# Kernel optimization log

Hardware: AMD Instinct MI355X
Metric: run time of the kernel (lower is better)

## Reference

```python
import jax, jax.numpy as jnp
import numpy as np

N_NODES = 100000
N_EDGES = 1600000
F_IN = 256
F_OUT = 128


def setup_inputs() -> dict:
    key = jax.random.key(0)
    k1, k2, k3, k4, k5 = jax.random.split(key, 5)
    x = jax.random.normal(k1, (N_NODES, F_IN), dtype=jnp.float32)
    edge_src = jax.random.randint(k2, (N_EDGES,), 0, N_NODES, dtype=jnp.int64)
    edge_dst = jax.random.randint(k3, (N_EDGES,), 0, N_NODES, dtype=jnp.int64)
    edge_vals = jax.random.uniform(k4, (N_EDGES,), dtype=jnp.float32)
    kernel = jax.random.normal(k5, (F_IN, F_OUT), dtype=jnp.float32) * (1.0 / np.sqrt(F_IN))
    bias = jnp.zeros((F_OUT,), dtype=jnp.float32)
    return {"x": x, "edge_src": edge_src, "edge_dst": edge_dst,
            "edge_vals": edge_vals, "kernel": kernel, "bias": bias}


def reference(x, edge_src, edge_dst, edge_vals, kernel, bias):
    # h = x @ kernel  (dense feature transform), [N, F_OUT]
    h = x @ kernel
    # output = adj @ h  (sparse aggregation over COO edges)
    # message for edge e: adj[dst, src] * h[src]
    msg = h[edge_src] * edge_vals[:, None]          # [E, F_OUT]
    out = jax.ops.segment_sum(msg, edge_dst, num_segments=N_NODES)
    return out + bias
```

## Files before the change

### kernel.cpp

```cpp
#include <hip/hip_runtime.h>

constexpr int F_IN  = 256;
constexpr int F_OUT = 128;

constexpr int BSHIFT = 6;
constexpr int SUPSH  = 5;
constexpr int NPSH   = BSHIFT + SUPSH;
constexpr int NPS    = 1 << NPSH;
constexpr int EPT    = 16;
constexpr int BATCH  = 256 * EPT;

typedef __attribute__((ext_vector_type(8))) short short8;
typedef __attribute__((ext_vector_type(4))) float f32x4;

__device__ __forceinline__ unsigned short f2bf(float f) {
    unsigned u = __float_as_uint(f);
    u += 0x7fffu + ((u >> 16) & 1u);
    return (unsigned short)(u >> 16);
}

__global__ void prep_wt_kernel(const float* __restrict__ W,
                               unsigned short* __restrict__ Wt,
                               int* __restrict__ cnt)
{
    int n = blockIdx.x;
    int k = threadIdx.x;
    int ks = k >> 5, kk = k & 31;
    Wt[((ks * F_OUT) + n) * 32 + kk] = f2bf(W[k * F_OUT + n]);
    if (blockIdx.x == 0 && threadIdx.x < 64) cnt[threadIdx.x] = 0;
}

#define BS_LD 40

__global__ __launch_bounds__(256) void gemm_mfma_kernel(
    const float* __restrict__ x, const unsigned short* __restrict__ Wt,
    unsigned short* __restrict__ h, int n_nodes)
{
    __shared__ unsigned short Bs[2][F_OUT * BS_LD];

    const int tid  = threadIdx.x;
    const int wave = tid >> 6;
    const int lane = tid & 63;
    const int m16  = lane & 15;
    const int quad = lane >> 4;
    const int k0q  = quad * 8;
    const int arow = blockIdx.x * 64 + wave * 16 + m16;
    const bool inb = arow < n_nodes;

    f32x4 acc[8];
    #pragma unroll
    for (int t = 0; t < 8; ++t) acc[t] = (f32x4)(0.f);

    {
        const uint4* wsrc = (const uint4*)Wt;
        #pragma unroll
        for (int p = 0; p < 2; ++p) {
            int c = p * 256 + tid;
            *(uint4*)&Bs[0][(c >> 2) * BS_LD + (c & 3) * 8] = wsrc[c];
        }
    }

    float4 a0 = make_float4(0.f,0.f,0.f,0.f), a1 = a0;
    if (inb) {
        a0 = *(const float4*)&x[(long long)arow * F_IN + k0q];
        a1 = *(const float4*)&x[(long long)arow * F_IN + k0q + 4];
    }
    __syncthreads();

    #pragma unroll
    for (int ks = 0; ks < 8; ++ks) {
        uint4 s0, s1;
        if (ks < 7) {
            const uint4* wsrc = (const uint4*)(Wt + (size_t)(ks + 1) * F_OUT * 32);
            s0 = wsrc[tid];
            s1 = wsrc[256 + tid];
        }

        short8 af;
        af[0] = (short)f2bf(a0.x); af[1] = (short)f2bf(a0.y);
        af[2] = (short)f2bf(a0.z); af[3] = (short)f2bf(a0.w);
        af[4] = (short)f2bf(a1.x); af[5] = (short)f2bf(a1.y);
        af[6] = (short)f2bf(a1.z); af[7] = (short)f2bf(a1.w);
        if (!inb) af = (short8)0;

        if (ks < 7 && inb) {
            int kn = (ks + 1) * 32 + k0q;
            a0 = *(const float4*)&x[(long long)arow * F_IN + kn];
            a1 = *(const float4*)&x[(long long)arow * F_IN + kn + 4];
        }

        #pragma unroll
        for (int t = 0; t < 8; ++t) {
            int n = t * 16 + m16;
            short8 bf = *(const short8*)&Bs[ks & 1][n * BS_LD + k0q];
            acc[t] = __builtin_amdgcn_mfma_f32_16x16x32_bf16(af, bf, acc[t], 0, 0, 0);
        }

        if (ks < 7) {
            *(uint4*)&Bs[(ks + 1) & 1][(tid >> 2) * BS_LD + (tid & 3) * 8] = s0;
            int c1 = 256 + tid;
            *(uint4*)&Bs[(ks + 1) & 1][(c1 >> 2) * BS_LD + (c1 & 3) * 8] = s1;
            __syncthreads();
        }
    }

    const int rbase = blockIdx.x * 64 + wave * 16 + quad * 4;
    #pragma unroll
    for (int r = 0; r < 4; ++r) {
        int grow = rbase + r;
        if (grow < n_nodes) {
            #pragma unroll
            for (int t = 0; t < 8; ++t)
                h[(long long)grow * F_OUT + t * 16 + m16] = f2bf(acc[t][r]);
        }
    }
}

__global__ __launch_bounds__(256) void hist_kernel(
    const int* __restrict__ dst, int* __restrict__ cnt, int n_edges)
{
    __shared__ int hs[64];
    const int tid = threadIdx.x;
    if (tid < 64) hs[tid] = 0;
    __syncthreads();
    for (int i = blockIdx.x * 256 + tid; i < n_edges; i += gridDim.x * 256)
        atomicAdd(&hs[dst[i] >> NPSH], 1);
    __syncthreads();
    if (tid < 64) {
        int v = hs[tid];
        if (v) atomicAdd(&cnt[tid], v);
    }
}

__global__ void scan_sup_kernel(const int* __restrict__ cnt,
                                int* __restrict__ super_start,
                                int* __restrict__ cursorA, int nsup)
{
    __shared__ int s[64];
    int t = threadIdx.x;
    s[t] = (t < nsup) ? cnt[t] : 0;
    __syncthreads();
    if (t == 0) {
        int run = 0;
        for (int i = 0; i < nsup; ++i) {
            super_start[i] = run; cursorA[i] = run; run += s[i];
        }
        super_start[nsup] = run;
    }
}

__global__ __launch_bounds__(256) void partition_a_kernel(
    const int* __restrict__ src, const int* __restrict__ dst,
    const float* __restrict__ vals, int* __restrict__ cursorA,
    uint2* __restrict__ payA, int n_edges)
{
    __shared__ int hist[64];
    __shared__ int base[64];
    const int tid = threadIdx.x;
    const int i0  = blockIdx.x * BATCH;

    if (tid < 64) hist[tid] = 0;
    __syncthreads();

    uint2 p[EPT];
    int   sb[EPT];
    int   rk[EPT];
    #pragma unroll
    for (int j = 0; j < EPT; ++j) {
        int i = i0 + j * 256 + tid;
        sb[j] = -1;
        if (i < n_edges) {
            int d = dst[i];
            p[j] = make_uint2((unsigned)src[i] | ((unsigned)(d & (NPS - 1)) << 17),
                              __float_as_uint(vals[i]));
            sb[j] = d >> NPSH;
            rk[j] = atomicAdd(&hist[sb[j]], 1);
        }
    }
    __syncthreads();
    if (tid < 64) { int v = hist[tid]; if (v) base[tid] = atomicAdd(&cursorA[tid], v); }
    __syncthreads();
    #pragma unroll
    for (int j = 0; j < EPT; ++j)
        if (sb[j] >= 0) payA[base[sb[j]] + rk[j]] = p[j];
}

__global__ __launch_bounds__(512) void sort_super_kernel(
    const uint2* __restrict__ payA, const int* __restrict__ super_start,
    uint2* __restrict__ sorted, int* __restrict__ offsets, int n_nodes)
{
    __shared__ int bins[NPS];
    __shared__ int bcur[NPS];
    __shared__ int ss[512];

    const int sp  = blockIdx.x;
    const int tid = threadIdx.x;
    const int lo  = super_start[sp];
    const int hi  = super_start[sp + 1];

    for (int i = tid; i < NPS; i += 512) bins[i] = 0;
    __syncthreads();

    {
        int e = lo + tid;
        for (; e + 3 * 512 < hi; e += 4 * 512) {
            unsigned x0 = payA[e].x, x1 = payA[e + 512].x,
                     x2 = payA[e + 1024].x, x3 = payA[e + 1536].x;
            atomicAdd(&bins[(x0 >> 17) & (NPS - 1)], 1);
            atomicAdd(&bins[(x1 >> 17) & (NPS - 1)], 1);
            atomicAdd(&bins[(x2 >> 17) & (NPS - 1)], 1);
            atomicAdd(&bins[(x3 >> 17) & (NPS - 1)], 1);
        }
        for (; e < hi; e += 512)
            atomicAdd(&bins[(payA[e].x >> 17) & (NPS - 1)], 1);
    }
    __syncthreads();

    const int b4 = tid * 4;
    int c0 = bins[b4], c1 = bins[b4 + 1], c2 = bins[b4 + 2], c3 = bins[b4 + 3];
    int tot = c0 + c1 + c2 + c3;
    ss[tid] = tot;
    __syncthreads();
    for (int off = 1; off < 512; off <<= 1) {
        int v = (tid >= off) ? ss[tid - off] : 0;
        __syncthreads();
        ss[tid] += v;
        __syncthreads();
    }
    int run = lo + ss[tid] - tot;
    bcur[b4]     = run;
    bcur[b4 + 1] = run + c0;
    bcur[b4 + 2] = run + c0 + c1;
    bcur[b4 + 3] = run + c0 + c1 + c2;
    __syncthreads();

    const int node0 = sp << NPSH;
    for (int i = tid; i < NPS; i += 512) {
        int nd = node0 + i;
        if (nd < n_nodes) offsets[nd] = bcur[i];
    }
    __syncthreads();

    {
        int e = lo + tid;
        for (; e + 3 * 512 < hi; e += 4 * 512) {
            uint2 p0 = payA[e], p1 = payA[e + 512], p2 = payA[e + 1024], p3 = payA[e + 1536];
            int q0 = atomicAdd(&bcur[(p0.x >> 17) & (NPS - 1)], 1);
            int q1 = atomicAdd(&bcur[(p1.x >> 17) & (NPS - 1)], 1);
            int q2 = atomicAdd(&bcur[(p2.x >> 17) & (NPS - 1)], 1);
            int q3 = atomicAdd(&bcur[(p3.x >> 17) & (NPS - 1)], 1);
            sorted[q0] = make_uint2(p0.x & 0x1FFFFu, p0.y);
            sorted[q1] = make_uint2(p1.x & 0x1FFFFu, p1.y);
            sorted[q2] = make_uint2(p2.x & 0x1FFFFu, p2.y);
            sorted[q3] = make_uint2(p3.x & 0x1FFFFu, p3.y);
        }
        for (; e < hi; e += 512) {
            uint2 p = payA[e];
            int q = atomicAdd(&bcur[(p.x >> 17) & (NPS - 1)], 1);
            sorted[q] = make_uint2(p.x & 0x1FFFFu, p.y);
        }
    }
}

__global__ __launch_bounds__(256) void gather_kernel(
    const unsigned short* __restrict__ h, const int* __restrict__ offsets,
    const uint2* __restrict__ sv, const float* __restrict__ bias,
    float* __restrict__ out, int n_nodes, int n_edges)
{
    int node = blockIdx.x * 4 + (threadIdx.x >> 6);
    if (node >= n_nodes) return;
    int lane = threadIdx.x & 63;
    int f = lane * 2;

    int start = offsets[node];
    int end   = (node + 1 < n_nodes) ? offsets[node + 1] : n_edges;

    float ax = 0.f, ay = 0.f;

    for (int e = start; e < end; e += 16) {
        uint2 p[16];
        #pragma unroll
        for (int j = 0; j < 16; ++j) {
            int ei = (e + j < end) ? e + j : end - 1;
            p[j] = sv[ei];
        }
        unsigned u[16];
        #pragma unroll
        for (int j = 0; j < 16; ++j)
            u[j] = *(const unsigned*)&h[(size_t)(p[j].x & 0x00FFFFFFu) * F_OUT + f];
        #pragma unroll
        for (int j = 0; j < 16; ++j) {
            float v = (e + j < end) ? __uint_as_float(p[j].y) : 0.f;
            ax += v * __uint_as_float(u[j] << 16);
            ay += v * __uint_as_float(u[j] & 0xffff0000u);
        }
    }

    float2 b = *(const float2*)&bias[f];
    *(float2*)&out[(size_t)node * F_OUT + f] = make_float2(ax + b.x, ay + b.y);
}

extern "C" void kernel_launch(void* const* d_in, const int* in_sizes, int n_in,
                              void* d_out, int out_size, void* d_ws, size_t ws_size,
                              hipStream_t stream)
{
    const float* x     = (const float*)d_in[0];
    const int*   esrc  = (const int*)d_in[1];
    const int*   edst  = (const int*)d_in[2];
    const float* evals = (const float*)d_in[3];
    const float* W     = (const float*)d_in[4];
    const float* bias  = (const float*)d_in[5];
    float*       out   = (float*)d_out;

    const int n_nodes = in_sizes[0] / F_IN;
    const int n_edges = in_sizes[1];
    const int nsup    = (n_nodes + NPS - 1) >> NPSH;

    auto align16 = [](size_t v) { return (v + 15) & ~(size_t)15; };
    char*  base = (char*)d_ws;
    size_t off  = 0;
    unsigned short* h  = (unsigned short*)(base + off); off = align16(off + (size_t)n_nodes * F_OUT * 2);
    unsigned short* Wt = (unsigned short*)(base + off); off = align16(off + (size_t)F_IN * F_OUT * 2);
    int*   cnt         = (int*)(base + off);   off = align16(off + (size_t)64 * 4);
    int*   super_start = (int*)(base + off);   off = align16(off + (size_t)(nsup + 1) * 4);
    int*   cursorA     = (int*)(base + off);   off = align16(off + (size_t)64 * 4);
    int*   offsets     = (int*)(base + off);   off = align16(off + (size_t)n_nodes * 4);
    uint2* payA        = (uint2*)(base + off); off = align16(off + (size_t)n_edges * 8);
    uint2* sorted      = (uint2*)(base + off); off = align16(off + (size_t)n_edges * 8);
    (void)ws_size;

    prep_wt_kernel<<<F_OUT, F_IN, 0, stream>>>(W, Wt, cnt);
    gemm_mfma_kernel<<<(n_nodes + 63) / 64, 256, 0, stream>>>(x, Wt, h, n_nodes);

    hist_kernel<<<256, 256, 0, stream>>>(edst, cnt, n_edges);
    scan_sup_kernel<<<1, 64, 0, stream>>>(cnt, super_start, cursorA, nsup);
    partition_a_kernel<<<(n_edges + BATCH - 1) / BATCH, 256, 0, stream>>>(
        esrc, edst, evals, cursorA, payA, n_edges);
    sort_super_kernel<<<nsup, 512, 0, stream>>>(
        payA, super_start, sorted, offsets, n_nodes);

    gather_kernel<<<(n_nodes + 3) / 4, 256, 0, stream>>>(
        h, offsets, sorted, bias, out, n_nodes, n_edges);
}
```

Before: 359.7 us.

## Single-buffer GEMM weight tile and split gather into three node-range launches

```diff
diff --git a/kernel.cpp b/kernel.cpp
--- a/kernel.cpp
+++ b/kernel.cpp
@@ -36,7 +36,7 @@
     const float* __restrict__ x, const unsigned short* __restrict__ Wt,
     unsigned short* __restrict__ h, int n_nodes)
 {
-    __shared__ unsigned short Bs[2][F_OUT * BS_LD];
+    __shared__ unsigned short Bs[F_OUT * BS_LD];
 
     const int tid  = threadIdx.x;
     const int wave = tid >> 6;
@@ -51,30 +51,22 @@
     #pragma unroll
     for (int t = 0; t < 8; ++t) acc[t] = (f32x4)(0.f);
 
-    {
-        const uint4* wsrc = (const uint4*)Wt;
-        #pragma unroll
-        for (int p = 0; p < 2; ++p) {
-            int c = p * 256 + tid;
-            *(uint4*)&Bs[0][(c >> 2) * BS_LD + (c & 3) * 8] = wsrc[c];
-        }
-    }
-
     float4 a0 = make_float4(0.f,0.f,0.f,0.f), a1 = a0;
     if (inb) {
         a0 = *(const float4*)&x[(long long)arow * F_IN + k0q];
         a1 = *(const float4*)&x[(long long)arow * F_IN + k0q + 4];
     }
-    __syncthreads();
-
-    #pragma unroll
+
     for (int ks = 0; ks < 8; ++ks) {
-        uint4 s0, s1;
-        if (ks < 7) {
-            const uint4* wsrc = (const uint4*)(Wt + (size_t)(ks + 1) * F_OUT * 32);
-            s0 = wsrc[tid];
-            s1 = wsrc[256 + tid];
-        }
+        const uint4* wsrc = (const uint4*)(Wt + (size_t)ks * F_OUT * 32);
+        #pragma unroll
+        for (int p = 0; p < 2; ++p) {
+            int c   = p * 256 + tid;
+            int row = c >> 2;
+            int o16 = c & 3;
+            *(uint4*)&Bs[row * BS_LD + o16 * 8] = wsrc[c];
+        }
+        __syncthreads();
 
         short8 af;
         af[0] = (short)f2bf(a0.x); af[1] = (short)f2bf(a0.y);
@@ -92,16 +84,10 @@
         #pragma unroll
         for (int t = 0; t < 8; ++t) {
             int n = t * 16 + m16;
-            short8 bf = *(const short8*)&Bs[ks & 1][n * BS_LD + k0q];
+            short8 bf = *(const short8*)&Bs[n * BS_LD + k0q];
             acc[t] = __builtin_amdgcn_mfma_f32_16x16x32_bf16(af, bf, acc[t], 0, 0, 0);
         }
-
-        if (ks < 7) {
-            *(uint4*)&Bs[(ks + 1) & 1][(tid >> 2) * BS_LD + (tid & 3) * 8] = s0;
-            int c1 = 256 + tid;
-            *(uint4*)&Bs[(ks + 1) & 1][(c1 >> 2) * BS_LD + (c1 & 3) * 8] = s1;
-            __syncthreads();
-        }
+        __syncthreads();
     }
 
     const int rbase = blockIdx.x * 64 + wave * 16 + quad * 4;
@@ -265,10 +251,11 @@
 __global__ __launch_bounds__(256) void gather_kernel(
     const unsigned short* __restrict__ h, const int* __restrict__ offsets,
     const uint2* __restrict__ sv, const float* __restrict__ bias,
-    float* __restrict__ out, int n_nodes, int n_edges)
-{
-    int node = blockIdx.x * 4 + (threadIdx.x >> 6);
-    if (node >= n_nodes) return;
+    float* __restrict__ out, int node_lo, int node_hi,
+    int n_nodes, int n_edges)
+{
+    int node = node_lo + blockIdx.x * 4 + (threadIdx.x >> 6);
+    if (node >= node_hi) return;
     int lane = threadIdx.x & 63;
     int f = lane * 2;
 
@@ -339,6 +326,12 @@
     sort_super_kernel<<<nsup, 512, 0, stream>>>(
         payA, super_start, sorted, offsets, n_nodes);
 
-    gather_kernel<<<(n_nodes + 3) / 4, 256, 0, stream>>>(
-        h, offsets, sorted, bias, out, n_nodes, n_edges);
-}
+    const int third = ((n_nodes / 3) + 63) & ~63;
+    const int r0 = third, r1 = 2 * third;
+    gather_kernel<<<(r0 + 3) / 4, 256, 0, stream>>>(
+        h, offsets, sorted, bias, out, 0, r0, n_nodes, n_edges);
+    gather_kernel<<<(r0 + 3) / 4, 256, 0, stream>>>(
+        h, offsets, sorted, bias, out, r0, r1, n_nodes, n_edges);
+    gather_kernel<<<(n_nodes - r1 + 3) / 4, 256, 0, stream>>>(
+        h, offsets, sorted, bias, out, r1, n_nodes, n_nodes, n_edges);
+}
```

New measurement: 374.1 us. +4.0%, slower.
